# Performance work log

Measured on AMD Instinct MI355X. Metric: run time of the kernel, lower is better.

The kernel has to match this reference:

```python
import jax, jax.numpy as jnp
import numpy as np


def _bd(x, W, b):
    # block-diagonal linear: x [B, D] -> [B, Dout], W [H, D/H, Dout/H], b [Dout]
    B, D = x.shape
    H = W.shape[0]
    y = jnp.einsum('bhi,hio->bho', x.reshape(B, H, D // H), W)
    return y.reshape(B, -1) + b


def setup_inputs() -> dict:
    key = jax.random.key(0)
    ks = jax.random.split(key, 16)
    B, D, H = 8192, 1024, 8
    U = int(D * 4 / 3)  # 1365
    d = D // H          # 128
    s = 0.05
    f32 = jnp.float32
    return {
        'x': jax.random.normal(ks[0], (B, D), f32),
        'h_prev': jax.random.normal(ks[1], (B, D), f32),
        'c_prev': jax.random.normal(ks[2], (B, D), f32),
        'n_prev': jax.random.uniform(ks[3], (B, D), f32) + 0.5,  # positive normalizer state
        'm_prev': jax.random.normal(ks[4], (B, D), f32),
        'ln_g': jnp.ones((D,), f32),
        'ln_b': jnp.zeros((D,), f32),
        'conv_w': jax.random.normal(ks[5], (1, 1, 4), f32) * 0.5,
        'conv_b': jax.random.normal(ks[6], (1,), f32) * 0.1,
        'W': jax.random.normal(ks[7], (4, H, d, d), f32) * s,   # gates z,i,f,o input projections
        'bW': jax.random.normal(ks[8], (4, D), f32) * s,
        'R': jax.random.normal(ks[9], (4, H, d, d), f32) * s,   # gates z,i,f,o recurrent projections
        'bR': jax.random.normal(ks[10], (4, D), f32) * s,
        'upl_w': jax.random.normal(ks[11], (D, U), f32) * s,
        'upl_b': jnp.zeros((U,), f32),
        'upr_w': jax.random.normal(ks[12], (D, U), f32) * s,
        'upr_b': jnp.zeros((U,), f32),
        'down_w': jax.random.normal(ks[13], (U, D), f32) * s,
        'down_b': jnp.zeros((D,), f32),
    }


def reference(x, h_prev, c_prev, n_prev, m_prev, ln_g, ln_b, conv_w, conv_b,
              W, bW, R, bR, upl_w, upl_b, upr_w, upr_b, down_w, down_b):
    # LayerNorm over feature dim (eps matches torch default 1e-5)
    mu = jnp.mean(x, axis=-1, keepdims=True)
    var = jnp.var(x, axis=-1, keepdims=True)
    x_norm = (x - mu) * jax.lax.rsqrt(var + 1e-5) * ln_g + ln_b
    # causal conv1d along the feature axis: kernel 4, left-pad 3 (Conv1d(1,1,4))
    conv = jax.lax.conv_general_dilated(
        x_norm[:, None, :], conv_w, window_strides=(1,), padding=[(3, 0)],
        dimension_numbers=('NCH', 'OIH', 'NCH'))[:, 0, :] + conv_b
    x_conv = jax.nn.silu(conv)
    # block-diagonal gate pre-activations (gate order in W/R stacks: z, i, f, o)
    z = jnp.tanh(_bd(x, W[0], bW[0]) + _bd(h_prev, R[0], bR[0]))
    o = jax.nn.sigmoid(_bd(x, W[3], bW[3]) + _bd(h_prev, R[3], bR[3]))
    i_tilde = _bd(x_conv, W[1], bW[1]) + _bd(h_prev, R[1], bR[1])
    f_tilde = _bd(x_conv, W[2], bW[2]) + _bd(h_prev, R[2], bR[2])
    # stabilized exp-max gating
    m_t = jnp.maximum(f_tilde + m_prev, i_tilde)
    i = jnp.exp(i_tilde - m_t)
    f = jnp.exp(f_tilde + m_prev - m_t)
    c_t = f * c_prev + i * z
    n_t = f * n_prev + i
    h_t = o * c_t / n_t
    # gated MLP (torch F.gelu default = exact erf gelu)
    left = h_t @ upl_w + upl_b
    right = jax.nn.gelu(h_t @ upr_w + upr_b, approximate=False)
    output = (left * right) @ down_w + down_b
    return (output, h_t, c_t, n_t, m_t)
```

## Files before the change

kernel.cpp:

```cpp
#include <hip/hip_runtime.h>
#include <hip/hip_bf16.h>

typedef __attribute__((ext_vector_type(8))) short s8v;
typedef __attribute__((ext_vector_type(4))) float f4v;
typedef unsigned short us4 __attribute__((ext_vector_type(4)));

#define NB 8192
#define ND 1024
#define NH 8
#define NU 1365
#define NUP 1408
#define GK 384
#define GN 512
static const size_t BD = (size_t)NB * ND;

#define WS_AG   ((size_t)0)
#define WS_G    ((size_t)50331648)
#define WS_HBF  ((size_t)73400320)
#define WS_WG   ((size_t)90177536)
#define WS_ULR  ((size_t)93323264)
#define WS_DWNT ((size_t)99090432)

__device__ __forceinline__ void gload16(const void* g, void* l) {
  __builtin_amdgcn_global_load_lds((const __attribute__((address_space(1))) void*)g,
                                   (__attribute__((address_space(3))) void*)l, 16, 0, 0);
}
__device__ __forceinline__ unsigned short tobf(float f) {
  unsigned int u = __float_as_uint(f);
  unsigned int r = (u + 0x7FFFu + ((u >> 16) & 1u)) >> 16;
  return (unsigned short)r;
}
__device__ __forceinline__ float frombf(unsigned short u) {
  return __uint_as_float(((unsigned int)u) << 16);
}
__device__ __forceinline__ float frcp(float x) { return __builtin_amdgcn_rcpf(x); }
__device__ __forceinline__ float fsigm(float x) { return frcp(1.f + __expf(-x)); }
__device__ __forceinline__ float ftanh(float x) {
  float e = __expf(2.f * x);
  return 1.f - 2.f * frcp(e + 1.f);
}
__device__ __forceinline__ f4v mfma16(s8v a, s8v b, f4v c) {
  return __builtin_amdgcn_mfma_f32_16x16x32_bf16(a, b, c, 0, 0, 0);
}

__global__ __launch_bounds__(256) void prep_kernel(
    const float* __restrict__ W, const float* __restrict__ R,
    const float* __restrict__ upl, const float* __restrict__ upr,
    const float* __restrict__ dwn,
    unsigned short* __restrict__ Wg, unsigned short* __restrict__ ULR,
    unsigned short* __restrict__ Dt) {
  long long idx = (long long)blockIdx.x * 256 + threadIdx.x;
  const long long N1 = (long long)4096 * GK;
  const long long N3 = (long long)2 * NUP * ND;
  const long long N2 = (long long)NUP * ND;
  if (idx < N1) {
    int c = (int)(idx / GK), k = (int)(idx % GK);
    int j = c & 15, g = (c >> 4) & 3, cgrp = (c >> 6) & 7, h = c >> 9;
    int o = cgrp * 16 + j;
    float v = 0.f;
    if (k < 128) {
      if (g == 0 || g == 3) v = W[(((size_t)g * NH + h) * 128 + k) * 128 + o];
    } else if (k < 256) {
      if (g == 1 || g == 2) v = W[(((size_t)g * NH + h) * 128 + (k - 128)) * 128 + o];
    } else {
      v = R[(((size_t)g * NH + h) * 128 + (k - 256)) * 128 + o];
    }
    Wg[idx] = tobf(v);
    return;
  }
  idx -= N1;
  if (idx < N3) {
    int r = (int)(idx / ND), k = (int)(idx % ND);
    int o = (r >> 4) & 1;
    int gcol = (r >> 5) * 16 + (r & 15);
    float v = 0.f;
    if (gcol < NU) v = o ? upr[(size_t)k * NU + gcol] : upl[(size_t)k * NU + gcol];
    ULR[idx] = tobf(v);
    return;
  }
  idx -= N3;
  if (idx < N2) { int n = (int)(idx / NUP), k = (int)(idx % NUP);
    Dt[idx] = (k < NU) ? tobf(dwn[(size_t)k * ND + n]) : 0; return; }
}

__global__ __launch_bounds__(256) void norm_conv(
    const float* __restrict__ x, const float* __restrict__ hp,
    const float* __restrict__ lg, const float* __restrict__ lb,
    const float* __restrict__ cw, const float* __restrict__ cb,
    unsigned short* __restrict__ Ag) {
  const int b = blockIdx.x, tid = threadIdx.x;
  const int lane = tid & 63, wv = tid >> 6;
  __shared__ float xs[1024];
  __shared__ float red[8];
  const int d0 = tid * 4;
  float4 xv = *(const float4*)(x + (size_t)b * ND + d0);
  float s = xv.x + xv.y + xv.z + xv.w;
  float ss = xv.x * xv.x + xv.y * xv.y + xv.z * xv.z + xv.w * xv.w;
#pragma unroll
  for (int o = 32; o; o >>= 1) { s += __shfl_down(s, o); ss += __shfl_down(ss, o); }
  if (lane == 0) { red[wv] = s; red[4 + wv] = ss; }
  __syncthreads();
  float S = red[0] + red[1] + red[2] + red[3];
  float SS = red[4] + red[5] + red[6] + red[7];
  float mu = S * (1.f / ND);
  float var = SS * (1.f / ND) - mu * mu;
  float rstd = rsqrtf(var + 1e-5f);
  float xn[4];
#pragma unroll
  for (int t = 0; t < 4; ++t) {
    float xx = (&xv.x)[t];
    xn[t] = (xx - mu) * rstd * lg[d0 + t] + lb[d0 + t];
    xs[d0 + t] = xn[t];
  }
  __syncthreads();
  float w0 = cw[0], w1 = cw[1], w2 = cw[2], w3 = cw[3], cbv = cb[0];
  float cv[4];
#pragma unroll
  for (int t = 0; t < 4; ++t) {
    int d = d0 + t;
    float a = cbv + w3 * xs[d];
    if (d >= 1) a += w2 * xs[d - 1];
    if (d >= 2) a += w1 * xs[d - 2];
    if (d >= 3) a += w0 * xs[d - 3];
    cv[t] = a * fsigm(a);
  }
  float4 hv = *(const float4*)(hp + (size_t)b * ND + d0);
  const int h = d0 >> 7, j = d0 & 127;
  us4 px, pc, ph;
#pragma unroll
  for (int t = 0; t < 4; ++t) { px[t] = tobf((&xv.x)[t]); pc[t] = tobf(cv[t]); ph[t] = tobf((&hv.x)[t]); }
  size_t base = (size_t)b * 3072 + (size_t)h * 384 + j;
  *(us4*)(Ag + base) = px;
  *(us4*)(Ag + base + 128) = pc;
  *(us4*)(Ag + base + 256) = ph;
}

__global__ __launch_bounds__(256) void gate_fused(
    const unsigned short* __restrict__ Ag, const unsigned short* __restrict__ Wg,
    const float* __restrict__ bW, const float* __restrict__ bR,
    const float* __restrict__ cp, const float* __restrict__ np_,
    const float* __restrict__ mp,
    float* __restrict__ dout, unsigned short* __restrict__ Hb) {
  __shared__ short As[128 * 32];
  __shared__ short Bs[128 * 32];
  const int tid = threadIdx.x, lane = tid & 63, wv = tid >> 6;
  const int wm = wv >> 1, wn = wv & 1;
  const int row0 = blockIdx.x * 128;
  const int p = blockIdx.y;
  const int h = blockIdx.z;
  const int srow = wv * 32 + (lane >> 2), scol = (lane & 3) * 8;
  const unsigned short* At = Ag + (size_t)h * 384;
  const unsigned short* Bt = Wg + ((size_t)h * 512 + (size_t)p * 128) * GK;
  const int cgrp = p * 2 + wn;
  const int gcol = h * 128 + cgrp * 16 + (lane & 15);
  float pc_[16], pn_[16], pm_[16];
#pragma unroll
  for (int m = 0; m < 4; ++m)
#pragma unroll
    for (int r = 0; r < 4; ++r) {
      const size_t idx = (size_t)(row0 + wm * 64 + m * 16 + (lane >> 4) * 4 + r) * ND + gcol;
      pc_[m * 4 + r] = cp[idx];
      pn_[m * 4 + r] = np_[idx];
      pm_[m * 4 + r] = mp[idx];
    }
  f4v acc[4][4] = {};
#pragma unroll
  for (int kt = 0; kt < 12; ++kt) {
    const int k0 = kt * 32;
    gload16(At + (size_t)(row0 + srow) * 3072 + k0 + scol, (char*)As + wv * 2048);
    gload16(At + (size_t)(row0 + srow + 16) * 3072 + k0 + scol, (char*)As + wv * 2048 + 1024);
    gload16(Bt + (size_t)srow * GK + k0 + scol, (char*)Bs + wv * 2048);
    gload16(Bt + (size_t)(srow + 16) * GK + k0 + scol, (char*)Bs + wv * 2048 + 1024);
    __syncthreads();
    s8v a[4];
#pragma unroll
    for (int m = 0; m < 4; ++m)
      a[m] = *(const s8v*)&As[(wm * 64 + m * 16 + (lane & 15)) * 32 + (lane >> 4) * 8];
#pragma unroll
    for (int g = 0; g < 4; ++g) {
      const bool active = (kt >= 8) || (kt < 4 ? (g == 0 || g == 3) : (g == 1 || g == 2));
      if (active) {
        s8v b = *(const s8v*)&Bs[(wn * 64 + g * 16 + (lane & 15)) * 32 + (lane >> 4) * 8];
#pragma unroll
        for (int m = 0; m < 4; ++m) acc[m][g] = mfma16(a[m], b, acc[m][g]);
      }
    }
    __syncthreads();
  }
  const float Bz = bW[gcol] + bR[gcol];
  const float Bi = bW[ND + gcol] + bR[ND + gcol];
  const float Bf = bW[2 * ND + gcol] + bR[2 * ND + gcol];
  const float Bo = bW[3 * ND + gcol] + bR[3 * ND + gcol];
#pragma unroll
  for (int m = 0; m < 4; ++m) {
    const int rbase = row0 + wm * 64 + m * 16 + (lane >> 4) * 4;
#pragma unroll
    for (int r = 0; r < 4; ++r) {
      const int e = m * 4 + r;
      const size_t idx = (size_t)(rbase + r) * ND + gcol;
      float zt = ftanh(acc[m][0][r] + Bz);
      float it = acc[m][1][r] + Bi;
      float ft = acc[m][2][r] + Bf;
      float ot = fsigm(acc[m][3][r] + Bo);
      float mv = pm_[e];
      float mt = fmaxf(ft + mv, it);
      float ii = __expf(it - mt);
      float ff = __expf(ft + mv - mt);
      float ct = ff * pc_[e] + ii * zt;
      float nt = ff * pn_[e] + ii;
      float ht = ot * ct * frcp(nt);
      dout[BD + idx] = ht;
      dout[2 * BD + idx] = ct;
      dout[3 * BD + idx] = nt;
      dout[4 * BD + idx] = mt;
      Hb[idx] = tobf(ht);
    }
  }
}

__global__ __launch_bounds__(256) void up_gemm(
    const unsigned short* __restrict__ A, const unsigned short* __restrict__ ULR,
    const float* __restrict__ lbias, const float* __restrict__ rbias,
    unsigned short* __restrict__ G) {
  __shared__ short As[4096];
  __shared__ short Bs[4096];
  const int tid = threadIdx.x, lane = tid & 63, wv = tid >> 6;
  const int wm = wv >> 1, wn = wv & 1;
  const int bid = blockIdx.x;
  const int swz = (bid & 7) * 176 + (bid >> 3);
  const int row0 = (swz / 22) * 128, n0 = (swz % 22) * 128;
  const int srow = wv * 32 + (lane >> 2), scol = (lane & 3) * 8;
  f4v acc[4][4] = {};
  for (int kt = 0; kt < 32; ++kt) {
    const int k0 = kt * 32;
    gload16(A + (size_t)(row0 + srow) * 1024 + k0 + scol, (char*)As + wv * 2048);
    gload16(A + (size_t)(row0 + srow + 16) * 1024 + k0 + scol, (char*)As + wv * 2048 + 1024);
    gload16(ULR + (size_t)(n0 + srow) * 1024 + k0 + scol, (char*)Bs + wv * 2048);
    gload16(ULR + (size_t)(n0 + srow + 16) * 1024 + k0 + scol, (char*)Bs + wv * 2048 + 1024);
    __syncthreads();
    s8v a[4], b[4];
#pragma unroll
    for (int m = 0; m < 4; ++m) a[m] = *(const s8v*)&As[(wm * 64 + m * 16 + (lane & 15)) * 32 + (lane >> 4) * 8];
#pragma unroll
    for (int n = 0; n < 4; ++n) b[n] = *(const s8v*)&Bs[(wn * 64 + n * 16 + (lane & 15)) * 32 + (lane >> 4) * 8];
#pragma unroll
    for (int m = 0; m < 4; ++m)
#pragma unroll
      for (int n = 0; n < 4; ++n) acc[m][n] = mfma16(a[m], b[n], acc[m][n]);
    __syncthreads();
  }
  const int gb = (n0 >> 1) + wn * 32;
#pragma unroll
  for (int m = 0; m < 4; ++m) {
    const int row = row0 + wm * 64 + m * 16 + (lane >> 4) * 4;
#pragma unroll
    for (int p = 0; p < 2; ++p) {
      const int gcol = gb + p * 16 + (lane & 15);
      const bool ok = gcol < NU;
      const float bl_ = ok ? lbias[gcol] : 0.f;
      const float br_ = ok ? rbias[gcol] : 0.f;
#pragma unroll
      for (int r = 0; r < 4; ++r) {
        float L = acc[m][2 * p][r] + bl_;
        float Rv = acc[m][2 * p + 1][r] + br_;
        float ge = 0.5f * Rv * (1.f + erff(Rv * 0.70710678118654752f));
        G[(size_t)(row + r) * NUP + gcol] = ok ? tobf(L * ge) : (unsigned short)0;
      }
    }
  }
}

__global__ __launch_bounds__(256) void down_gemm(
    const unsigned short* __restrict__ A, const unsigned short* __restrict__ Bt,
    const float* __restrict__ dbias, float* __restrict__ out) {
  __shared__ short As[4096];
  __shared__ short Bs[4096];
  const int tid = threadIdx.x, lane = tid & 63, wv = tid >> 6;
  const int wm = wv >> 1, wn = wv & 1;
  const int bid = blockIdx.x;
  const int swz = (bid & 7) * 64 + (bid >> 3);
  const int row0 = (swz >> 3) * 128, n0 = (swz & 7) * 128;
  const int srow = wv * 32 + (lane >> 2), scol = (lane & 3) * 8;
  f4v acc[4][4] = {};
  for (int kt = 0; kt < NUP / 32; ++kt) {
    const int k0 = kt * 32;
    gload16(A + (size_t)(row0 + srow) * NUP + k0 + scol, (char*)As + wv * 2048);
    gload16(A + (size_t)(row0 + srow + 16) * NUP + k0 + scol, (char*)As + wv * 2048 + 1024);
    gload16(Bt + (size_t)(n0 + srow) * NUP + k0 + scol, (char*)Bs + wv * 2048);
    gload16(Bt + (size_t)(n0 + srow + 16) * NUP + k0 + scol, (char*)Bs + wv * 2048 + 1024);
    __syncthreads();
    s8v a[4], b[4];
#pragma unroll
    for (int m = 0; m < 4; ++m) a[m] = *(const s8v*)&As[(wm * 64 + m * 16 + (lane & 15)) * 32 + (lane >> 4) * 8];
#pragma unroll
    for (int n = 0; n < 4; ++n) b[n] = *(const s8v*)&Bs[(wn * 64 + n * 16 + (lane & 15)) * 32 + (lane >> 4) * 8];
#pragma unroll
    for (int m = 0; m < 4; ++m)
#pragma unroll
      for (int n = 0; n < 4; ++n) acc[m][n] = mfma16(a[m], b[n], acc[m][n]);
    __syncthreads();
  }
#pragma unroll
  for (int m = 0; m < 4; ++m) {
    const int row = row0 + wm * 64 + m * 16 + (lane >> 4) * 4;
#pragma unroll
    for (int n = 0; n < 4; ++n) {
      const int col = n0 + wn * 64 + n * 16 + (lane & 15);
      const float bias = dbias[col];
#pragma unroll
      for (int r = 0; r < 4; ++r)
        out[(size_t)(row + r) * ND + col] = acc[m][n][r] + bias;
    }
  }
}

extern "C" void kernel_launch(void* const* d_in, const int* in_sizes, int n_in,
                              void* d_out, int out_size, void* d_ws, size_t ws_size,
                              hipStream_t stream) {
  const float* x    = (const float*)d_in[0];
  const float* hp   = (const float*)d_in[1];
  const float* cp   = (const float*)d_in[2];
  const float* np_  = (const float*)d_in[3];
  const float* mp   = (const float*)d_in[4];
  const float* lg   = (const float*)d_in[5];
  const float* lb   = (const float*)d_in[6];
  const float* cw   = (const float*)d_in[7];
  const float* cb   = (const float*)d_in[8];
  const float* W    = (const float*)d_in[9];
  const float* bW   = (const float*)d_in[10];
  const float* R    = (const float*)d_in[11];
  const float* bR   = (const float*)d_in[12];
  const float* upl  = (const float*)d_in[13];
  const float* uplb = (const float*)d_in[14];
  const float* upr  = (const float*)d_in[15];
  const float* uprb = (const float*)d_in[16];
  const float* dwn  = (const float*)d_in[17];
  const float* dwnb = (const float*)d_in[18];
  float* out = (float*)d_out;
  char* ws = (char*)d_ws;
  unsigned short* Ag  = (unsigned short*)(ws + WS_AG);
  unsigned short* G   = (unsigned short*)(ws + WS_G);
  unsigned short* Hb  = (unsigned short*)(ws + WS_HBF);
  unsigned short* Wg  = (unsigned short*)(ws + WS_WG);
  unsigned short* ULR = (unsigned short*)(ws + WS_ULR);
  unsigned short* Dt  = (unsigned short*)(ws + WS_DWNT);

  prep_kernel<<<23040, 256, 0, stream>>>(W, R, upl, upr, dwn, Wg, ULR, Dt);
  norm_conv<<<NB, 256, 0, stream>>>(x, hp, lg, lb, cw, cb, Ag);
  gate_fused<<<dim3(64, 4, 8), 256, 0, stream>>>(Ag, Wg, bW, bR, cp, np_, mp, out, Hb);
  up_gemm<<<1408, 256, 0, stream>>>(Hb, ULR, uplb, uprb, G);
  down_gemm<<<512, 256, 0, stream>>>(G, Dt, dwnb, out);
}
```

Baseline: 255.8 us.

## Rewrite MLP GEMMs as 8-wave 256x128 tiles with double-buffered swizzled LDS

The up and down projection GEMMs move from 4-wave 128x128 tiles with a single LDS buffer and K=32 steps to 8-wave 256x128 tiles. These use K=64 steps, double-buffered LDS, an XOR swizzle and a four-phase schedule that prefetches the next tile's halves during MFMA phases. The goal is to hide global-load latency, remove the two full syncs per K step, cut LDS bank conflicts and raise reuse per block. In exchange it uses more LDS per block (96KB), so fewer blocks fit per CU, and the fine-grained manual waitcnt/barrier logic is fragile. Grid sizes are halved to match the larger tiles.

```diff
diff --git a/kernel.cpp b/kernel.cpp
--- a/kernel.cpp
+++ b/kernel.cpp
@@ -4,6 +4,7 @@
 typedef __attribute__((ext_vector_type(8))) short s8v;
 typedef __attribute__((ext_vector_type(4))) float f4v;
 typedef unsigned short us4 __attribute__((ext_vector_type(4)));
+typedef unsigned short ushort_t;
 
 #define NB 8192
 #define ND 1024
@@ -29,9 +30,6 @@
   unsigned int u = __float_as_uint(f);
   unsigned int r = (u + 0x7FFFu + ((u >> 16) & 1u)) >> 16;
   return (unsigned short)r;
-}
-__device__ __forceinline__ float frombf(unsigned short u) {
-  return __uint_as_float(((unsigned int)u) << 16);
 }
 __device__ __forceinline__ float frcp(float x) { return __builtin_amdgcn_rcpf(x); }
 __device__ __forceinline__ float fsigm(float x) { return frcp(1.f + __expf(-x)); }
@@ -218,98 +216,153 @@
   }
 }
 
-__global__ __launch_bounds__(256) void up_gemm(
+
+__device__ __forceinline__ void stage_a_half(
+    const unsigned short* __restrict__ Ab, int ldA, int row0, int t, int mh,
+    short* lds, int wid, int lane) {
+#pragma unroll
+  for (int q = 0; q < 2; ++q) {
+    const int ldsrow = mh * 128 + (wid * 2 + q) * 8;
+    const int g = (lane & 7) ^ (((lane >> 5) & 1) << 1);
+    gload16(Ab + (size_t)(row0 + ldsrow + (lane >> 3)) * ldA + t * 64 + g * 8,
+            lds + ldsrow * 64);
+  }
+}
+__device__ __forceinline__ void stage_b_half(
+    const unsigned short* __restrict__ Bb, int ldB, int n0, int t, int nh,
+    short* lds, int wid, int lane) {
+  const int ldsrow = nh * 64 + wid * 8;
+  const int g = (lane & 7) ^ (((lane >> 5) & 1) << 1);
+  gload16(Bb + (size_t)(n0 + ldsrow + (lane >> 3)) * ldB + t * 64 + g * 8,
+          lds + ldsrow * 64);
+}
+
+#define DS_A(MH)                                                                 \
+  _Pragma("unroll") for (int mf = 0; mf < 2; ++mf)                               \
+  _Pragma("unroll") for (int kk = 0; kk < 2; ++kk) {                             \
+    const int rr_ = (MH) * 128 + (wid >> 1) * 32 + mf * 16 + (lane & 15);        \
+    const int ix_ = (rr_ * 64 + kk * 32 + ((lane >> 4) & 3) * 8) ^               \
+                    (((rr_ >> 2) & 1) << 4);                                     \
+    av[mf][kk] = *(const s8v*)&As[cur][ix_];                                     \
+  }
+#define DS_B(NH)                                                                 \
+  _Pragma("unroll") for (int nf = 0; nf < 2; ++nf)                               \
+  _Pragma("unroll") for (int kk = 0; kk < 2; ++kk) {                             \
+    const int rr_ = (NH) * 64 + (wid & 1) * 32 + nf * 16 + (lane & 15);          \
+    const int ix_ = (rr_ * 64 + kk * 32 + ((lane >> 4) & 3) * 8) ^               \
+                    (((rr_ >> 2) & 1) << 4);                                     \
+    bv[nf][kk] = *(const s8v*)&Bs[cur][ix_];                                     \
+  }
+#define PHASE_MM(MH, NH)                                                         \
+  __builtin_amdgcn_s_barrier();                                                  \
+  asm volatile("s_waitcnt lgkmcnt(0)" ::: "memory");                             \
+  __builtin_amdgcn_sched_barrier(0);                                             \
+  __builtin_amdgcn_s_setprio(1);                                                 \
+  _Pragma("unroll") for (int kk = 0; kk < 2; ++kk)                               \
+  _Pragma("unroll") for (int mf = 0; mf < 2; ++mf)                               \
+  _Pragma("unroll") for (int nf = 0; nf < 2; ++nf)                               \
+    acc[(MH) * 2 + mf][(NH) * 2 + nf] =                                          \
+        mfma16(av[mf][kk], bv[nf][kk], acc[(MH) * 2 + mf][(NH) * 2 + nf]);       \
+  __builtin_amdgcn_s_setprio(0);                                                 \
+  __builtin_amdgcn_sched_barrier(0);
+
+#define GEMM8_BODY(Aptr, LDA, Bptr, LDB, NT)                                     \
+  stage_a_half(Aptr, LDA, row0, 0, 0, &As[0][0], wid, lane);                     \
+  stage_b_half(Bptr, LDB, n0, 0, 0, &Bs[0][0], wid, lane);                       \
+  stage_a_half(Aptr, LDA, row0, 0, 1, &As[0][0], wid, lane);                     \
+  stage_b_half(Bptr, LDB, n0, 0, 1, &Bs[0][0], wid, lane);                       \
+  stage_b_half(Bptr, LDB, n0, 1, 0, &Bs[1][0], wid, lane);                       \
+  stage_a_half(Aptr, LDA, row0, 1, 1, &As[1][0], wid, lane);                     \
+  asm volatile("s_waitcnt vmcnt(3)" ::: "memory");                               \
+  __builtin_amdgcn_s_barrier();                                                  \
+  for (int u = 0; u < (NT); ++u) {                                               \
+    const int cur = u & 1, nxt = cur ^ 1;                                        \
+    s8v av[2][2], bv[2][2];                                                      \
+                       \
+    DS_A(0); DS_B(0);                                                            \
+    if (u + 1 < (NT)) {                                                          \
+      stage_a_half(Aptr, LDA, row0, u + 1, 0, &As[nxt][0], wid, lane);           \
+      stage_b_half(Bptr, LDB, n0, u + 1, 1, &Bs[nxt][0], wid, lane);             \
+    }                                                                            \
+    PHASE_MM(0, 0);                                                              \
+    __builtin_amdgcn_s_barrier();                                                \
+                                                                 \
+    DS_A(1);                                                                     \
+    PHASE_MM(1, 0);                                                              \
+    __builtin_amdgcn_s_barrier();                                                \
+           \
+    DS_B(1);                                                                     \
+    if (u + 2 < (NT)) stage_b_half(Bptr, LDB, n0, u + 2, 0, &Bs[cur][0], wid, lane); \
+    PHASE_MM(1, 1);                                                              \
+    __builtin_amdgcn_s_barrier();                                                \
+                            \
+    DS_A(0);                                                                     \
+    if (u + 2 < (NT)) stage_a_half(Aptr, LDA, row0, u + 2, 1, &As[cur][0], wid, lane); \
+    PHASE_MM(0, 1);                                                              \
+    if (u + 2 < (NT)) { asm volatile("s_waitcnt vmcnt(3)" ::: "memory"); }       \
+    else              { asm volatile("s_waitcnt vmcnt(0)" ::: "memory"); }       \
+    __builtin_amdgcn_s_barrier();                                                \
+  }
+
+__global__ __launch_bounds__(512) void up8_gemm(
     const unsigned short* __restrict__ A, const unsigned short* __restrict__ ULR,
     const float* __restrict__ lbias, const float* __restrict__ rbias,
     unsigned short* __restrict__ G) {
-  __shared__ short As[4096];
-  __shared__ short Bs[4096];
-  const int tid = threadIdx.x, lane = tid & 63, wv = tid >> 6;
-  const int wm = wv >> 1, wn = wv & 1;
+  __shared__ short As[2][16384];
+  __shared__ short Bs[2][8192];
+  const int tid = threadIdx.x, lane = tid & 63, wid = tid >> 6;
   const int bid = blockIdx.x;
-  const int swz = (bid & 7) * 176 + (bid >> 3);
-  const int row0 = (swz / 22) * 128, n0 = (swz % 22) * 128;
-  const int srow = wv * 32 + (lane >> 2), scol = (lane & 3) * 8;
+  const int swz = (bid & 7) * 88 + (bid >> 3);
+  const int row0 = (swz / 22) * 256, n0 = (swz % 22) * 128;
   f4v acc[4][4] = {};
-  for (int kt = 0; kt < 32; ++kt) {
-    const int k0 = kt * 32;
-    gload16(A + (size_t)(row0 + srow) * 1024 + k0 + scol, (char*)As + wv * 2048);
-    gload16(A + (size_t)(row0 + srow + 16) * 1024 + k0 + scol, (char*)As + wv * 2048 + 1024);
-    gload16(ULR + (size_t)(n0 + srow) * 1024 + k0 + scol, (char*)Bs + wv * 2048);
-    gload16(ULR + (size_t)(n0 + srow + 16) * 1024 + k0 + scol, (char*)Bs + wv * 2048 + 1024);
-    __syncthreads();
-    s8v a[4], b[4];
-#pragma unroll
-    for (int m = 0; m < 4; ++m) a[m] = *(const s8v*)&As[(wm * 64 + m * 16 + (lane & 15)) * 32 + (lane >> 4) * 8];
-#pragma unroll
-    for (int n = 0; n < 4; ++n) b[n] = *(const s8v*)&Bs[(wn * 64 + n * 16 + (lane & 15)) * 32 + (lane >> 4) * 8];
-#pragma unroll
-    for (int m = 0; m < 4; ++m)
-#pragma unroll
-      for (int n = 0; n < 4; ++n) acc[m][n] = mfma16(a[m], b[n], acc[m][n]);
-    __syncthreads();
-  }
-  const int gb = (n0 >> 1) + wn * 32;
-#pragma unroll
-  for (int m = 0; m < 4; ++m) {
-    const int row = row0 + wm * 64 + m * 16 + (lane >> 4) * 4;
-#pragma unroll
-    for (int p = 0; p < 2; ++p) {
-      const int gcol = gb + p * 16 + (lane & 15);
+  GEMM8_BODY(A, 1024, ULR, 1024, 16);
+#pragma unroll
+  for (int mh = 0; mh < 2; ++mh)
+#pragma unroll
+  for (int mf = 0; mf < 2; ++mf) {
+    const int rbase = row0 + mh * 128 + (wid >> 1) * 32 + mf * 16 + (lane >> 4) * 4;
+#pragma unroll
+    for (int nh = 0; nh < 2; ++nh) {
+      const int gcol = ((n0 + nh * 64 + (wid & 1) * 32) >> 1) + (lane & 15);
       const bool ok = gcol < NU;
       const float bl_ = ok ? lbias[gcol] : 0.f;
       const float br_ = ok ? rbias[gcol] : 0.f;
 #pragma unroll
       for (int r = 0; r < 4; ++r) {
-        float L = acc[m][2 * p][r] + bl_;
-        float Rv = acc[m][2 * p + 1][r] + br_;
+        float L = acc[mh * 2 + mf][nh * 2 + 0][r] + bl_;
+        float Rv = acc[mh * 2 + mf][nh * 2 + 1][r] + br_;
         float ge = 0.5f * Rv * (1.f + erff(Rv * 0.70710678118654752f));
-        G[(size_t)(row + r) * NUP + gcol] = ok ? tobf(L * ge) : (unsigned short)0;
+        G[(size_t)(rbase + r) * NUP + gcol] = ok ? tobf(L * ge) : (unsigned short)0;
       }
     }
   }
 }
 
-__global__ __launch_bounds__(256) void down_gemm(
+__global__ __launch_bounds__(512) void down8_gemm(
     const unsigned short* __restrict__ A, const unsigned short* __restrict__ Bt,
     const float* __restrict__ dbias, float* __restrict__ out) {
-  __shared__ short As[4096];
-  __shared__ short Bs[4096];
-  const int tid = threadIdx.x, lane = tid & 63, wv = tid >> 6;
-  const int wm = wv >> 1, wn = wv & 1;
+  __shared__ short As[2][16384];
+  __shared__ short Bs[2][8192];
+  const int tid = threadIdx.x, lane = tid & 63, wid = tid >> 6;
   const int bid = blockIdx.x;
-  const int swz = (bid & 7) * 64 + (bid >> 3);
-  const int row0 = (swz >> 3) * 128, n0 = (swz & 7) * 128;
-  const int srow = wv * 32 + (lane >> 2), scol = (lane & 3) * 8;
+  const int swz = (bid & 7) * 32 + (bid >> 3);
+  const int row0 = (swz >> 3) * 256, n0 = (swz & 7) * 128;
   f4v acc[4][4] = {};
-  for (int kt = 0; kt < NUP / 32; ++kt) {
-    const int k0 = kt * 32;
-    gload16(A + (size_t)(row0 + srow) * NUP + k0 + scol, (char*)As + wv * 2048);
-    gload16(A + (size_t)(row0 + srow + 16) * NUP + k0 + scol, (char*)As + wv * 2048 + 1024);
-    gload16(Bt + (size_t)(n0 + srow) * NUP + k0 + scol, (char*)Bs + wv * 2048);
-    gload16(Bt + (size_t)(n0 + srow + 16) * NUP + k0 + scol, (char*)Bs + wv * 2048 + 1024);
-    __syncthreads();
-    s8v a[4], b[4];
-#pragma unroll
-    for (int m = 0; m < 4; ++m) a[m] = *(const s8v*)&As[(wm * 64 + m * 16 + (lane & 15)) * 32 + (lane >> 4) * 8];
-#pragma unroll
-    for (int n = 0; n < 4; ++n) b[n] = *(const s8v*)&Bs[(wn * 64 + n * 16 + (lane & 15)) * 32 + (lane >> 4) * 8];
-#pragma unroll
-    for (int m = 0; m < 4; ++m)
-#pragma unroll
-      for (int n = 0; n < 4; ++n) acc[m][n] = mfma16(a[m], b[n], acc[m][n]);
-    __syncthreads();
-  }
-#pragma unroll
-  for (int m = 0; m < 4; ++m) {
-    const int row = row0 + wm * 64 + m * 16 + (lane >> 4) * 4;
-#pragma unroll
-    for (int n = 0; n < 4; ++n) {
-      const int col = n0 + wn * 64 + n * 16 + (lane & 15);
+  GEMM8_BODY(A, NUP, Bt, NUP, 22);
+#pragma unroll
+  for (int mh = 0; mh < 2; ++mh)
+#pragma unroll
+  for (int mf = 0; mf < 2; ++mf) {
+    const int rbase = row0 + mh * 128 + (wid >> 1) * 32 + mf * 16 + (lane >> 4) * 4;
+#pragma unroll
+    for (int nh = 0; nh < 2; ++nh)
+#pragma unroll
+    for (int nf = 0; nf < 2; ++nf) {
+      const int col = n0 + nh * 64 + (wid & 1) * 32 + nf * 16 + (lane & 15);
       const float bias = dbias[col];
 #pragma unroll
       for (int r = 0; r < 4; ++r)
-        out[(size_t)(row + r) * ND + col] = acc[m][n][r] + bias;
+        out[(size_t)(rbase + r) * ND + col] = acc[mh * 2 + mf][nh * 2 + nf][r] + bias;
     }
   }
 }
@@ -348,6 +401,6 @@
   prep_kernel<<<23040, 256, 0, stream>>>(W, R, upl, upr, dwn, Wg, ULR, Dt);
   norm_conv<<<NB, 256, 0, stream>>>(x, hp, lg, lb, cw, cb, Ag);
   gate_fused<<<dim3(64, 4, 8), 256, 0, stream>>>(Ag, Wg, bW, bR, cp, np_, mp, out, Hb);
-  up_gemm<<<1408, 256, 0, stream>>>(Hb, ULR, uplb, uprb, G);
-  down_gemm<<<512, 256, 0, stream>>>(G, Dt, dwnb, out);
-}
+  up8_gemm<<<704, 512, 0, stream>>>(Hb, ULR, uplb, uprb, G);
+  down8_gemm<<<256, 512, 0, stream>>>(G, Dt, dwnb, out);
+}
```

Measured after the change: 278.0 us. 1.09x slower.

## Triple-buffer LDS tiles with async prefetch in all three GEMM kernels

Applied to the files above, without the earlier changes.

Replaces the single-buffered load/sync/compute/sync loop in gate_fused, up_gemm and down_gemm with a three-stage ring of LDS buffers. Tiles are prefetched two iterations ahead and completion is tracked with explicit vmcnt waits plus one barrier per iteration. The goal is to hide global-to-LDS latency behind MFMA work and halve the barriers. In exchange, LDS use per block triples to 48KB, which may reduce occupancy, and correctness now depends on hand-written waitcnt counts matching the four loads issued per stage.

```diff
diff --git a/kernel.cpp b/kernel.cpp
--- a/kernel.cpp
+++ b/kernel.cpp
@@ -29,9 +29,6 @@
   unsigned int u = __float_as_uint(f);
   unsigned int r = (u + 0x7FFFu + ((u >> 16) & 1u)) >> 16;
   return (unsigned short)r;
-}
-__device__ __forceinline__ float frombf(unsigned short u) {
-  return __uint_as_float(((unsigned int)u) << 16);
 }
 __device__ __forceinline__ float frcp(float x) { return __builtin_amdgcn_rcpf(x); }
 __device__ __forceinline__ float fsigm(float x) { return frcp(1.f + __expf(-x)); }
@@ -141,8 +138,8 @@
     const float* __restrict__ cp, const float* __restrict__ np_,
     const float* __restrict__ mp,
     float* __restrict__ dout, unsigned short* __restrict__ Hb) {
-  __shared__ short As[128 * 32];
-  __shared__ short Bs[128 * 32];
+  __shared__ short As[3][4096];
+  __shared__ short Bs[3][4096];
   const int tid = threadIdx.x, lane = tid & 63, wv = tid >> 6;
   const int wm = wv >> 1, wn = wv & 1;
   const int row0 = blockIdx.x * 128;
@@ -163,30 +160,40 @@
       pn_[m * 4 + r] = np_[idx];
       pm_[m * 4 + r] = mp[idx];
     }
+#define STGG(bb, kt_)                                                                   \
+  do {                                                                                  \
+    const int k0_ = (kt_) * 32;                                                         \
+    gload16(At + (size_t)(row0 + srow) * 3072 + k0_ + scol, (char*)As[bb] + wv * 2048); \
+    gload16(At + (size_t)(row0 + srow + 16) * 3072 + k0_ + scol,                        \
+            (char*)As[bb] + wv * 2048 + 1024);                                          \
+    gload16(Bt + (size_t)srow * GK + k0_ + scol, (char*)Bs[bb] + wv * 2048);            \
+    gload16(Bt + (size_t)(srow + 16) * GK + k0_ + scol,                                 \
+            (char*)Bs[bb] + wv * 2048 + 1024);                                          \
+  } while (0)
   f4v acc[4][4] = {};
-#pragma unroll
+  STGG(0, 0);
+  STGG(1, 1);
   for (int kt = 0; kt < 12; ++kt) {
-    const int k0 = kt * 32;
-    gload16(At + (size_t)(row0 + srow) * 3072 + k0 + scol, (char*)As + wv * 2048);
-    gload16(At + (size_t)(row0 + srow + 16) * 3072 + k0 + scol, (char*)As + wv * 2048 + 1024);
-    gload16(Bt + (size_t)srow * GK + k0 + scol, (char*)Bs + wv * 2048);
-    gload16(Bt + (size_t)(srow + 16) * GK + k0 + scol, (char*)Bs + wv * 2048 + 1024);
-    __syncthreads();
+    const int cur = kt % 3;
+    if (kt < 11) asm volatile("s_waitcnt vmcnt(4)" ::: "memory");
+    else         asm volatile("s_waitcnt vmcnt(0)" ::: "memory");
+    asm volatile("s_barrier" ::: "memory");
+    if (kt + 2 < 12) STGG((kt + 2) % 3, kt + 2);
     s8v a[4];
 #pragma unroll
     for (int m = 0; m < 4; ++m)
-      a[m] = *(const s8v*)&As[(wm * 64 + m * 16 + (lane & 15)) * 32 + (lane >> 4) * 8];
+      a[m] = *(const s8v*)&As[cur][(wm * 64 + m * 16 + (lane & 15)) * 32 + (lane >> 4) * 8];
 #pragma unroll
     for (int g = 0; g < 4; ++g) {
       const bool active = (kt >= 8) || (kt < 4 ? (g == 0 || g == 3) : (g == 1 || g == 2));
       if (active) {
-        s8v b = *(const s8v*)&Bs[(wn * 64 + g * 16 + (lane & 15)) * 32 + (lane >> 4) * 8];
+        s8v b = *(const s8v*)&Bs[cur][(wn * 64 + g * 16 + (lane & 15)) * 32 + (lane >> 4) * 8];
 #pragma unroll
         for (int m = 0; m < 4; ++m) acc[m][g] = mfma16(a[m], b, acc[m][g]);
       }
     }
-    __syncthreads();
-  }
+  }
+#undef STGG
   const float Bz = bW[gcol] + bR[gcol];
   const float Bi = bW[ND + gcol] + bR[ND + gcol];
   const float Bf = bW[2 * ND + gcol] + bR[2 * ND + gcol];
@@ -222,33 +229,46 @@
     const unsigned short* __restrict__ A, const unsigned short* __restrict__ ULR,
     const float* __restrict__ lbias, const float* __restrict__ rbias,
     unsigned short* __restrict__ G) {
-  __shared__ short As[4096];
-  __shared__ short Bs[4096];
+  __shared__ short As[3][4096];
+  __shared__ short Bs[3][4096];
   const int tid = threadIdx.x, lane = tid & 63, wv = tid >> 6;
   const int wm = wv >> 1, wn = wv & 1;
   const int bid = blockIdx.x;
   const int swz = (bid & 7) * 176 + (bid >> 3);
   const int row0 = (swz / 22) * 128, n0 = (swz % 22) * 128;
   const int srow = wv * 32 + (lane >> 2), scol = (lane & 3) * 8;
+#define STGU(bb, kt_)                                                                     \
+  do {                                                                                    \
+    const int k0_ = (kt_) * 32;                                                           \
+    gload16(A + (size_t)(row0 + srow) * 1024 + k0_ + scol, (char*)As[bb] + wv * 2048);    \
+    gload16(A + (size_t)(row0 + srow + 16) * 1024 + k0_ + scol,                           \
+            (char*)As[bb] + wv * 2048 + 1024);                                            \
+    gload16(ULR + (size_t)(n0 + srow) * 1024 + k0_ + scol, (char*)Bs[bb] + wv * 2048);    \
+    gload16(ULR + (size_t)(n0 + srow + 16) * 1024 + k0_ + scol,                           \
+            (char*)Bs[bb] + wv * 2048 + 1024);                                            \
+  } while (0)
   f4v acc[4][4] = {};
+  STGU(0, 0);
+  STGU(1, 1);
   for (int kt = 0; kt < 32; ++kt) {
-    const int k0 = kt * 32;
-    gload16(A + (size_t)(row0 + srow) * 1024 + k0 + scol, (char*)As + wv * 2048);
-    gload16(A + (size_t)(row0 + srow + 16) * 1024 + k0 + scol, (char*)As + wv * 2048 + 1024);
-    gload16(ULR + (size_t)(n0 + srow) * 1024 + k0 + scol, (char*)Bs + wv * 2048);
-    gload16(ULR + (size_t)(n0 + srow + 16) * 1024 + k0 + scol, (char*)Bs + wv * 2048 + 1024);
-    __syncthreads();
+    const int cur = kt % 3;
+    if (kt < 31) asm volatile("s_waitcnt vmcnt(4)" ::: "memory");
+    else         asm volatile("s_waitcnt vmcnt(0)" ::: "memory");
+    asm volatile("s_barrier" ::: "memory");
+    if (kt + 2 < 32) STGU((kt + 2) % 3, kt + 2);
     s8v a[4], b[4];
 #pragma unroll
-    for (int m = 0; m < 4; ++m) a[m] = *(const s8v*)&As[(wm * 64 + m * 16 + (lane & 15)) * 32 + (lane >> 4) * 8];
-#pragma unroll
-    for (int n = 0; n < 4; ++n) b[n] = *(const s8v*)&Bs[(wn * 64 + n * 16 + (lane & 15)) * 32 + (lane >> 4) * 8];
+    for (int m = 0; m < 4; ++m)
+      a[m] = *(const s8v*)&As[cur][(wm * 64 + m * 16 + (lane & 15)) * 32 + (lane >> 4) * 8];
+#pragma unroll
+    for (int n = 0; n < 4; ++n)
+      b[n] = *(const s8v*)&Bs[cur][(wn * 64 + n * 16 + (lane & 15)) * 32 + (lane >> 4) * 8];
 #pragma unroll
     for (int m = 0; m < 4; ++m)
 #pragma unroll
       for (int n = 0; n < 4; ++n) acc[m][n] = mfma16(a[m], b[n], acc[m][n]);
-    __syncthreads();
-  }
+  }
+#undef STGU
   const int gb = (n0 >> 1) + wn * 32;
 #pragma unroll
   for (int m = 0; m < 4; ++m) {
@@ -273,33 +293,47 @@
 __global__ __launch_bounds__(256) void down_gemm(
     const unsigned short* __restrict__ A, const unsigned short* __restrict__ Bt,
     const float* __restrict__ dbias, float* __restrict__ out) {
-  __shared__ short As[4096];
-  __shared__ short Bs[4096];
+  __shared__ short As[3][4096];
+  __shared__ short Bs[3][4096];
   const int tid = threadIdx.x, lane = tid & 63, wv = tid >> 6;
   const int wm = wv >> 1, wn = wv & 1;
   const int bid = blockIdx.x;
   const int swz = (bid & 7) * 64 + (bid >> 3);
   const int row0 = (swz >> 3) * 128, n0 = (swz & 7) * 128;
   const int srow = wv * 32 + (lane >> 2), scol = (lane & 3) * 8;
+  const int NT = NUP / 32;
+#define STGD(bb, kt_)                                                                     \
+  do {                                                                                    \
+    const int k0_ = (kt_) * 32;                                                           \
+    gload16(A + (size_t)(row0 + srow) * NUP + k0_ + scol, (char*)As[bb] + wv * 2048);     \
+    gload16(A + (size_t)(row0 + srow + 16) * NUP + k0_ + scol,                            \
+            (char*)As[bb] + wv * 2048 + 1024);                                            \
+    gload16(Bt + (size_t)(n0 + srow) * NUP + k0_ + scol, (char*)Bs[bb] + wv * 2048);      \
+    gload16(Bt + (size_t)(n0 + srow + 16) * NUP + k0_ + scol,                             \
+            (char*)Bs[bb] + wv * 2048 + 1024);                                            \
+  } while (0)
   f4v acc[4][4] = {};
-  for (int kt = 0; kt < NUP / 32; ++kt) {
-    const int k0 = kt * 32;
-    gload16(A + (size_t)(row0 + srow) * NUP + k0 + scol, (char*)As + wv * 2048);
-    gload16(A + (size_t)(row0 + srow + 16) * NUP + k0 + scol, (char*)As + wv * 2048 + 1024);
-    gload16(Bt + (size_t)(n0 + srow) * NUP + k0 + scol, (char*)Bs + wv * 2048);
-    gload16(Bt + (size_t)(n0 + srow + 16) * NUP + k0 + scol, (char*)Bs + wv * 2048 + 1024);
-    __syncthreads();
+  STGD(0, 0);
+  STGD(1, 1);
+  for (int kt = 0; kt < NT; ++kt) {
+    const int cur = kt % 3;
+    if (kt < NT - 1) asm volatile("s_waitcnt vmcnt(4)" ::: "memory");
+    else             asm volatile("s_waitcnt vmcnt(0)" ::: "memory");
+    asm volatile("s_barrier" ::: "memory");
+    if (kt + 2 < NT) STGD((kt + 2) % 3, kt + 2);
     s8v a[4], b[4];
 #pragma unroll
-    for (int m = 0; m < 4; ++m) a[m] = *(const s8v*)&As[(wm * 64 + m * 16 + (lane & 15)) * 32 + (lane >> 4) * 8];
-#pragma unroll
-    for (int n = 0; n < 4; ++n) b[n] = *(const s8v*)&Bs[(wn * 64 + n * 16 + (lane & 15)) * 32 + (lane >> 4) * 8];
+    for (int m = 0; m < 4; ++m)
+      a[m] = *(const s8v*)&As[cur][(wm * 64 + m * 16 + (lane & 15)) * 32 + (lane >> 4) * 8];
+#pragma unroll
+    for (int n = 0; n < 4; ++n)
+      b[n] = *(const s8v*)&Bs[cur][(wn * 64 + n * 16 + (lane & 15)) * 32 + (lane >> 4) * 8];
 #pragma unroll
     for (int m = 0; m < 4; ++m)
 #pragma unroll
       for (int n = 0; n < 4; ++n) acc[m][n] = mfma16(a[m], b[n], acc[m][n]);
-    __syncthreads();
-  }
+  }
+#undef STGD
 #pragma unroll
   for (int m = 0; m < 4; ++m) {
     const int row = row0 + wm * 64 + m * 16 + (lane >> 4) * 4;
```

Measured after the change: 264.8 us. 3.5% more time.
